# Performance work log

Hardware: AMD Instinct MI355X
Metric: run time of the kernel (lower is better)

The kernel has to match this reference:

```python
import jax, jax.numpy as jnp
import numpy as np

B, H, S, D = 1, 16, 4096, 64

def setup_inputs() -> dict:
    key = jax.random.key(0)
    kq, kk, kv = jax.random.split(key, 3)
    q = jax.random.normal(kq, (B, H, S, D), dtype=jnp.float32)
    k = jax.random.normal(kk, (B, H, S, D), dtype=jnp.float32)
    v = jax.random.normal(kv, (B, H, S, D), dtype=jnp.float32)
    return {"q": q, "k": k, "v": v}

def reference(q, k, v):
    # attn = q @ k^T  -> [B,H,S,S]; output = attn @ v -> [B,H,S,D]
    attn = jnp.einsum('bhqd,bhkd->bhqk', q, k)
    out = jnp.einsum('bhqk,bhkd->bhqd', attn, v)
    return out
```

## Files before the change

kernel.cpp:

```cpp
#include <hip/hip_runtime.h>
#include <stddef.h>


#define SLEN 4096
#define DIM  64
#define NH   16
#define CH   32
#define RPC  (SLEN / CH)

typedef float f4v __attribute__((ext_vector_type(4)));

__global__ __launch_bounds__(256) void kvT_partial(const float* __restrict__ K,
                                                   const float* __restrict__ V,
                                                   float* __restrict__ P) {
    const int c = blockIdx.x;
    const int h = blockIdx.y;
    const int t = threadIdx.x;
    const int i = t >> 4;
    const int j = t & 15;

    __shared__ float Ks[32][64];
    __shared__ float Vs[32][64];

    const f4v* K4 = (const f4v*)(K + ((size_t)h * SLEN + (size_t)c * RPC) * DIM);
    const f4v* V4 = (const f4v*)(V + ((size_t)h * SLEN + (size_t)c * RPC) * DIM);

    float acc[4][4] = {{0.f,0.f,0.f,0.f},{0.f,0.f,0.f,0.f},
                       {0.f,0.f,0.f,0.f},{0.f,0.f,0.f,0.f}};

    f4v kst[2], vst[2];
    #pragma unroll
    for (int u = 0; u < 2; ++u) {
        int idx = u * 256 + t, row = idx >> 4, c4 = idx & 15;
        kst[u] = K4[row * 16 + c4];
        vst[u] = V4[row * 16 + c4];
    }

    for (int tile = 0; tile < 4; ++tile) {
        __syncthreads();
        #pragma unroll
        for (int u = 0; u < 2; ++u) {
            int idx = u * 256 + t, row = idx >> 4, c4 = idx & 15;
            *(f4v*)&Ks[row][c4 * 4] = kst[u];
            *(f4v*)&Vs[row][c4 * 4] = vst[u];
        }
        __syncthreads();

        if (tile < 3) {
            #pragma unroll
            for (int u = 0; u < 2; ++u) {
                int idx = u * 256 + t, row = idx >> 4, c4 = idx & 15;
                kst[u] = K4[((tile + 1) * 32 + row) * 16 + c4];
                vst[u] = V4[((tile + 1) * 32 + row) * 16 + c4];
            }
        }

        #pragma unroll
        for (int s = 0; s < 32; ++s) {
            f4v kf = *(const f4v*)&Ks[s][i * 4];
            f4v vf = *(const f4v*)&Vs[s][j * 4];
            #pragma unroll
            for (int a = 0; a < 4; ++a)
                #pragma unroll
                for (int b = 0; b < 4; ++b)
                    acc[a][b] = fmaf(kf[a], vf[b], acc[a][b]);
        }
    }

    float* Pc = P + ((size_t)h * CH + c) * (DIM * DIM);
    #pragma unroll
    for (int a = 0; a < 4; ++a) {
        f4v r;
        r[0] = acc[a][0]; r[1] = acc[a][1]; r[2] = acc[a][2]; r[3] = acc[a][3];
        *(f4v*)&Pc[(i * 4 + a) * DIM + j * 4] = r;
    }
}

__global__ __launch_bounds__(256) void reduceM(const float* __restrict__ P,
                                               float* __restrict__ M) {
    const int q = blockIdx.x;
    const int h = blockIdx.y;
    const int t = threadIdx.x;
    const int off = q * 256 + t;

    const f4v* Ph = (const f4v*)(P + (size_t)h * CH * DIM * DIM);
    f4v sum; sum[0] = 0.f; sum[1] = 0.f; sum[2] = 0.f; sum[3] = 0.f;
    #pragma unroll
    for (int c = 0; c < CH; ++c) {
        f4v x = Ph[(size_t)c * (DIM * DIM / 4) + off];
        sum[0] += x[0]; sum[1] += x[1]; sum[2] += x[2]; sum[3] += x[3];
    }
    ((f4v*)(M + (size_t)h * DIM * DIM))[off] = sum;
}

__global__ __launch_bounds__(256) void qm_kernel(const float* __restrict__ Q,
                                                 const float* __restrict__ M,
                                                 float* __restrict__ O) {
    const int chunk = blockIdx.x;
    const int h     = blockIdx.y;
    const int t     = threadIdx.x;
    const int i     = t >> 4;
    const int j     = t & 15;

    __shared__ float Qs[64][68];
    __shared__ float Ms[64][64];

    const f4v* Q4 = (const f4v*)(Q + ((size_t)h * SLEN + (size_t)chunk * 64) * DIM);
    const f4v* M4 = (const f4v*)(M + (size_t)h * DIM * DIM);

    #pragma unroll
    for (int it = 0; it < 4; ++it) {
        int idx = it * 256 + t;
        int row = idx >> 4;
        int c4  = idx & 15;
        *(f4v*)&Qs[row][c4 * 4] = Q4[idx];
        *(f4v*)&Ms[row][c4 * 4] = M4[idx];
    }
    __syncthreads();

    float acc[4][4] = {{0.f,0.f,0.f,0.f},{0.f,0.f,0.f,0.f},
                       {0.f,0.f,0.f,0.f},{0.f,0.f,0.f,0.f}};

    for (int d0 = 0; d0 < DIM; d0 += 4) {
        f4v qf[4], mf[4];
        #pragma unroll
        for (int a = 0; a < 4; ++a)
            qf[a] = *(const f4v*)&Qs[i * 4 + a][d0];
        #pragma unroll
        for (int cc = 0; cc < 4; ++cc)
            mf[cc] = *(const f4v*)&Ms[d0 + cc][j * 4];
        #pragma unroll
        for (int a = 0; a < 4; ++a)
            #pragma unroll
            for (int cc = 0; cc < 4; ++cc)
                #pragma unroll
                for (int b = 0; b < 4; ++b)
                    acc[a][b] = fmaf(qf[a][cc], mf[cc][b], acc[a][b]);
    }

    f4v* O4 = (f4v*)O;
    #pragma unroll
    for (int a = 0; a < 4; ++a) {
        f4v res;
        res[0] = acc[a][0]; res[1] = acc[a][1]; res[2] = acc[a][2]; res[3] = acc[a][3];
        O4[((size_t)h * SLEN + (size_t)chunk * 64 + i * 4 + a) * (DIM / 4) + j] = res;
    }
}

extern "C" void kernel_launch(void* const* d_in, const int* in_sizes, int n_in,
                              void* d_out, int out_size, void* d_ws, size_t ws_size,
                              hipStream_t stream) {
    const float* q = (const float*)d_in[0];
    const float* k = (const float*)d_in[1];
    const float* v = (const float*)d_in[2];
    float* out = (float*)d_out;
    float* P = (float*)d_ws;
    float* M = P + (size_t)NH * CH * DIM * DIM;

    kvT_partial<<<dim3(CH, NH), 256, 0, stream>>>(k, v, P);
    reduceM<<<dim3(4, NH), 256, 0, stream>>>(P, M);
    qm_kernel<<<dim3(64, NH), 256, 0, stream>>>(q, M, out);
}
```

Measured before the change: 108.8 us.

## Enlarge per-thread register tiles and split-K across waves in KV^T and QM kernels

The KV^T partial kernel now gives each lane an 8x8 output tile, up from 4x4. Each of its four waves handles a quarter of the rows in every 64-row tile, and the four partial results are then combined through shared memory. The QM kernel now uses single-wave 64-thread blocks, also with 8x8 per-lane tiles, and stores Q in shared memory with an XOR swizzle to avoid bank conflicts. The goal is more FMAs per shared-memory load. The cost is higher register pressure, an extra in-block reduction step, and fewer threads per block in the QM kernel.

```diff
diff --git a/kernel.cpp b/kernel.cpp
--- a/kernel.cpp
+++ b/kernel.cpp
@@ -6,144 +6,175 @@
 #define DIM  64
 #define NH   16
 #define CH   32
-#define RPC  (SLEN / CH)
+#define RPC  128
 
 typedef float f4v __attribute__((ext_vector_type(4)));
 
 __global__ __launch_bounds__(256) void kvT_partial(const float* __restrict__ K,
                                                    const float* __restrict__ V,
                                                    float* __restrict__ P) {
-    const int c = blockIdx.x;
-    const int h = blockIdx.y;
-    const int t = threadIdx.x;
-    const int i = t >> 4;
-    const int j = t & 15;
+    const int c = blockIdx.x, h = blockIdx.y, t = threadIdx.x;
+    const int wave = t >> 6, lane = t & 63;
+    const int i = lane >> 3, j = lane & 7;
 
-    __shared__ float Ks[32][64];
-    __shared__ float Vs[32][64];
+    __shared__ float Ks[64][64];
+    __shared__ float Vs[64][64];
 
     const f4v* K4 = (const f4v*)(K + ((size_t)h * SLEN + (size_t)c * RPC) * DIM);
     const f4v* V4 = (const f4v*)(V + ((size_t)h * SLEN + (size_t)c * RPC) * DIM);
 
-    float acc[4][4] = {{0.f,0.f,0.f,0.f},{0.f,0.f,0.f,0.f},
-                       {0.f,0.f,0.f,0.f},{0.f,0.f,0.f,0.f}};
-
-    f4v kst[2], vst[2];
+    float acc[8][8];
     #pragma unroll
-    for (int u = 0; u < 2; ++u) {
-        int idx = u * 256 + t, row = idx >> 4, c4 = idx & 15;
-        kst[u] = K4[row * 16 + c4];
-        vst[u] = V4[row * 16 + c4];
+    for (int a = 0; a < 8; ++a) {
+        #pragma unroll
+        for (int b = 0; b < 8; ++b) acc[a][b] = 0.f;
     }
 
-    for (int tile = 0; tile < 4; ++tile) {
+    f4v kst[4], vst[4];
+    #pragma unroll
+    for (int u = 0; u < 4; ++u) { kst[u] = K4[u * 256 + t]; vst[u] = V4[u * 256 + t]; }
+
+    for (int tile = 0; tile < 2; ++tile) {
         __syncthreads();
         #pragma unroll
-        for (int u = 0; u < 2; ++u) {
+        for (int u = 0; u < 4; ++u) {
             int idx = u * 256 + t, row = idx >> 4, c4 = idx & 15;
             *(f4v*)&Ks[row][c4 * 4] = kst[u];
             *(f4v*)&Vs[row][c4 * 4] = vst[u];
         }
         __syncthreads();
-
-        if (tile < 3) {
+        if (tile == 0) {
             #pragma unroll
-            for (int u = 0; u < 2; ++u) {
-                int idx = u * 256 + t, row = idx >> 4, c4 = idx & 15;
-                kst[u] = K4[((tile + 1) * 32 + row) * 16 + c4];
-                vst[u] = V4[((tile + 1) * 32 + row) * 16 + c4];
+            for (int u = 0; u < 4; ++u) {
+                kst[u] = K4[1024 + u * 256 + t];
+                vst[u] = V4[1024 + u * 256 + t];
             }
         }
-
         #pragma unroll
-        for (int s = 0; s < 32; ++s) {
-            f4v kf = *(const f4v*)&Ks[s][i * 4];
-            f4v vf = *(const f4v*)&Vs[s][j * 4];
+        for (int s0 = 0; s0 < 16; ++s0) {
+            const int s = wave * 16 + s0;
+            float kf[8], vf[8];
+            *(f4v*)&kf[0] = *(const f4v*)&Ks[s][i * 8];
+            *(f4v*)&kf[4] = *(const f4v*)&Ks[s][i * 8 + 4];
+            *(f4v*)&vf[0] = *(const f4v*)&Vs[s][j * 8];
+            *(f4v*)&vf[4] = *(const f4v*)&Vs[s][j * 8 + 4];
             #pragma unroll
-            for (int a = 0; a < 4; ++a)
+            for (int a = 0; a < 8; ++a) {
                 #pragma unroll
-                for (int b = 0; b < 4; ++b)
+                for (int b = 0; b < 8; ++b)
                     acc[a][b] = fmaf(kf[a], vf[b], acc[a][b]);
+            }
         }
     }
 
+    __syncthreads();
+    float* M0 = &Ks[0][0];
+    float* M1 = &Vs[0][0];
+    if (wave == 0 || wave == 2) {
+        float* dst = (wave == 0) ? M0 : M1;
+        #pragma unroll
+        for (int r = 0; r < 8; ++r) {
+            #pragma unroll
+            for (int hh = 0; hh < 2; ++hh) {
+                f4v x; x[0]=acc[r][hh*4]; x[1]=acc[r][hh*4+1]; x[2]=acc[r][hh*4+2]; x[3]=acc[r][hh*4+3];
+                *(f4v*)&dst[(i * 8 + r) * 64 + j * 8 + hh * 4] = x;
+            }
+        }
+    }
+    __syncthreads();
+    if (wave == 1 || wave == 3) {
+        float* dst = (wave == 1) ? M0 : M1;
+        #pragma unroll
+        for (int r = 0; r < 8; ++r) {
+            #pragma unroll
+            for (int hh = 0; hh < 2; ++hh) {
+                f4v x = *(f4v*)&dst[(i * 8 + r) * 64 + j * 8 + hh * 4];
+                x[0]+=acc[r][hh*4]; x[1]+=acc[r][hh*4+1]; x[2]+=acc[r][hh*4+2]; x[3]+=acc[r][hh*4+3];
+                *(f4v*)&dst[(i * 8 + r) * 64 + j * 8 + hh * 4] = x;
+            }
+        }
+    }
+    __syncthreads();
     float* Pc = P + ((size_t)h * CH + c) * (DIM * DIM);
     #pragma unroll
-    for (int a = 0; a < 4; ++a) {
-        f4v r;
-        r[0] = acc[a][0]; r[1] = acc[a][1]; r[2] = acc[a][2]; r[3] = acc[a][3];
-        *(f4v*)&Pc[(i * 4 + a) * DIM + j * 4] = r;
+    for (int u = 0; u < 4; ++u) {
+        int idx = u * 256 + t;
+        f4v x = ((const f4v*)M0)[idx] + ((const f4v*)M1)[idx];
+        ((f4v*)Pc)[idx] = x;
     }
 }
 
 __global__ __launch_bounds__(256) void reduceM(const float* __restrict__ P,
                                                float* __restrict__ M) {
-    const int q = blockIdx.x;
-    const int h = blockIdx.y;
-    const int t = threadIdx.x;
+    const int q = blockIdx.x, h = blockIdx.y, t = threadIdx.x;
     const int off = q * 256 + t;
-
     const f4v* Ph = (const f4v*)(P + (size_t)h * CH * DIM * DIM);
-    f4v sum; sum[0] = 0.f; sum[1] = 0.f; sum[2] = 0.f; sum[3] = 0.f;
+    f4v sum; sum[0]=0.f; sum[1]=0.f; sum[2]=0.f; sum[3]=0.f;
     #pragma unroll
-    for (int c = 0; c < CH; ++c) {
-        f4v x = Ph[(size_t)c * (DIM * DIM / 4) + off];
-        sum[0] += x[0]; sum[1] += x[1]; sum[2] += x[2]; sum[3] += x[3];
-    }
+    for (int c = 0; c < CH; ++c) sum += Ph[(size_t)c * (DIM * DIM / 4) + off];
     ((f4v*)(M + (size_t)h * DIM * DIM))[off] = sum;
 }
 
-__global__ __launch_bounds__(256) void qm_kernel(const float* __restrict__ Q,
-                                                 const float* __restrict__ M,
-                                                 float* __restrict__ O) {
-    const int chunk = blockIdx.x;
-    const int h     = blockIdx.y;
-    const int t     = threadIdx.x;
-    const int i     = t >> 4;
-    const int j     = t & 15;
+__global__ __launch_bounds__(64) void qm_kernel(const float* __restrict__ Q,
+                                                const float* __restrict__ Mm,
+                                                float* __restrict__ O) {
+    const int chunk = blockIdx.x, h = blockIdx.y, lane = threadIdx.x;
+    const int i = lane >> 3, j = lane & 7;
 
-    __shared__ float Qs[64][68];
+    __shared__ float Qs[64][64];
     __shared__ float Ms[64][64];
 
     const f4v* Q4 = (const f4v*)(Q + ((size_t)h * SLEN + (size_t)chunk * 64) * DIM);
-    const f4v* M4 = (const f4v*)(M + (size_t)h * DIM * DIM);
+    const f4v* M4 = (const f4v*)(Mm + (size_t)h * DIM * DIM);
 
     #pragma unroll
-    for (int it = 0; it < 4; ++it) {
-        int idx = it * 256 + t;
-        int row = idx >> 4;
-        int c4  = idx & 15;
-        *(f4v*)&Qs[row][c4 * 4] = Q4[idx];
-        *(f4v*)&Ms[row][c4 * 4] = M4[idx];
+    for (int u = 0; u < 16; ++u) {
+        int idx = u * 64 + lane, row = idx >> 4, c4 = idx & 15;
+        int c4s = c4 ^ (row >> 3);
+        *(f4v*)&Qs[row][c4s * 4] = Q4[idx];
+        *(f4v*)&Ms[row][c4 * 4]  = M4[idx];
     }
     __syncthreads();
 
-    float acc[4][4] = {{0.f,0.f,0.f,0.f},{0.f,0.f,0.f,0.f},
-                       {0.f,0.f,0.f,0.f},{0.f,0.f,0.f,0.f}};
-
-    for (int d0 = 0; d0 < DIM; d0 += 4) {
-        f4v qf[4], mf[4];
+    float acc[8][8];
+    #pragma unroll
+    for (int a = 0; a < 8; ++a) {
         #pragma unroll
-        for (int a = 0; a < 4; ++a)
-            qf[a] = *(const f4v*)&Qs[i * 4 + a][d0];
-        #pragma unroll
-        for (int cc = 0; cc < 4; ++cc)
-            mf[cc] = *(const f4v*)&Ms[d0 + cc][j * 4];
-        #pragma unroll
-        for (int a = 0; a < 4; ++a)
-            #pragma unroll
-            for (int cc = 0; cc < 4; ++cc)
-                #pragma unroll
-                for (int b = 0; b < 4; ++b)
-                    acc[a][b] = fmaf(qf[a][cc], mf[cc][b], acc[a][b]);
+        for (int b = 0; b < 8; ++b) acc[a][b] = 0.f;
     }
 
-    f4v* O4 = (f4v*)O;
     #pragma unroll
-    for (int a = 0; a < 4; ++a) {
-        f4v res;
-        res[0] = acc[a][0]; res[1] = acc[a][1]; res[2] = acc[a][2]; res[3] = acc[a][3];
-        O4[((size_t)h * SLEN + (size_t)chunk * 64 + i * 4 + a) * (DIM / 4) + j] = res;
+    for (int d0 = 0; d0 < DIM; d0 += 4) {
+        const int c4q = d0 >> 2;
+        float qf[8][4];
+        #pragma unroll
+        for (int r = 0; r < 8; ++r)
+            *(f4v*)&qf[r][0] = *(const f4v*)&Qs[i * 8 + r][(c4q ^ i) * 4];
+        float mf[4][8];
+        #pragma unroll
+        for (int cc = 0; cc < 4; ++cc) {
+            *(f4v*)&mf[cc][0] = *(const f4v*)&Ms[d0 + cc][j * 8];
+            *(f4v*)&mf[cc][4] = *(const f4v*)&Ms[d0 + cc][j * 8 + 4];
+        }
+        #pragma unroll
+        for (int r = 0; r < 8; ++r) {
+            #pragma unroll
+            for (int cc = 0; cc < 4; ++cc) {
+                #pragma unroll
+                for (int b = 0; b < 8; ++b)
+                    acc[r][b] = fmaf(qf[r][cc], mf[cc][b], acc[r][b]);
+            }
+        }
+    }
+
+    float* Orow = O + ((size_t)h * SLEN + (size_t)chunk * 64) * DIM;
+    #pragma unroll
+    for (int r = 0; r < 8; ++r) {
+        #pragma unroll
+        for (int hh = 0; hh < 2; ++hh) {
+            f4v x; x[0]=acc[r][hh*4]; x[1]=acc[r][hh*4+1]; x[2]=acc[r][hh*4+2]; x[3]=acc[r][hh*4+3];
+            *(f4v*)&Orow[(i * 8 + r) * DIM + j * 8 + hh * 4] = x;
+        }
     }
 }
 
@@ -159,5 +190,5 @@
 
     kvT_partial<<<dim3(CH, NH), 256, 0, stream>>>(k, v, P);
     reduceM<<<dim3(4, NH), 256, 0, stream>>>(P, M);
-    qm_kernel<<<dim3(64, NH), 256, 0, stream>>>(q, M, out);
+    qm_kernel<<<dim3(SLEN / 64, NH), 64, 0, stream>>>(q, M, out);
 }
```

After: 111.6 us. +2.6%, slower.
